# Performance work log

Measured on AMD Instinct MI355X. Metric: run time of the kernel, lower is better.

Reference implementation:

```python
import jax, jax.numpy as jnp
import numpy as np

INPUT = 27
HIDDEN = 1


def setup_inputs() -> dict:
    key = jax.random.key(0)
    k_x, k_wih, k_whh, k_bih, k_bhh = jax.random.split(key, 5)
    s = 1.0 / np.sqrt(HIDDEN)  # PyTorch LSTM init range
    x = jax.random.normal(k_x, (2048, 512, INPUT), dtype=jnp.float32)
    W_ih = jax.random.uniform(k_wih, (4 * HIDDEN, INPUT), minval=-s, maxval=s, dtype=jnp.float32)
    W_hh = jax.random.uniform(k_whh, (4 * HIDDEN, HIDDEN), minval=-s, maxval=s, dtype=jnp.float32)
    b_ih = jax.random.uniform(k_bih, (4 * HIDDEN,), minval=-s, maxval=s, dtype=jnp.float32)
    b_hh = jax.random.uniform(k_bhh, (4 * HIDDEN,), minval=-s, maxval=s, dtype=jnp.float32)
    return {"x": x, "W_ih": W_ih, "W_hh": W_hh, "b_ih": b_ih, "b_hh": b_hh}


def reference(x, W_ih, W_hh, b_ih, b_hh):
    # x: (T, B, 27). Single-layer LSTM, hidden_size=1, PyTorch gate order i,f,g,o.
    T, B, _ = x.shape
    H = HIDDEN
    # Precompute the input projection for all timesteps: (T, B, 4H)
    x_proj = jnp.einsum('tbi,gi->tbg', x, W_ih) + b_ih + b_hh

    def step(carry, xp_t):
        h, c = carry  # (B, H) each
        gates = xp_t + h @ W_hh.T  # (B, 4H)
        i = jax.nn.sigmoid(gates[:, 0 * H:1 * H])
        f = jax.nn.sigmoid(gates[:, 1 * H:2 * H])
        g = jnp.tanh(gates[:, 2 * H:3 * H])
        o = jax.nn.sigmoid(gates[:, 3 * H:4 * H])
        c_new = f * c + i * g
        h_new = o * jnp.tanh(c_new)
        return (h_new, c_new), h_new

    h0 = jnp.zeros((B, H), dtype=x.dtype)
    c0 = jnp.zeros((B, H), dtype=x.dtype)
    _, hs = jax.lax.scan(step, (h0, c0), x_proj)
    return hs  # (T, B, H)
```

## Files before the change

kernel.cpp:

```cpp
#include <hip/hip_runtime.h>

#define T_LEN 2048
#define B_SZ  512
#define NIN   27

__device__ __forceinline__ float fast_exp2(float x) { return __builtin_amdgcn_exp2f(x); }
__device__ __forceinline__ float fast_rcp(float x)  { return __builtin_amdgcn_rcpf(x); }

#define L2E 1.4426950408889634f

__global__ __launch_bounds__(256) void lstm_proj(const float* __restrict__ x,
                                                 const float* __restrict__ Wih,
                                                 const float* __restrict__ bih,
                                                 const float* __restrict__ bhh,
                                                 float4* __restrict__ A) {
    __shared__ float xs[256 * NIN];
    const int tid  = threadIdx.x;
    const size_t pos0 = (size_t)blockIdx.x * 256;

    const float4* src4 = (const float4*)(x + pos0 * NIN);
    float4* lds4 = (float4*)xs;
#pragma unroll
    for (int i = 0; i < 6; ++i) lds4[tid + i * 256] = src4[tid + i * 256];
    {
        int idx = tid + 6 * 256;
        if (idx < (256 * NIN) / 4) lds4[idx] = src4[idx];
    }

    float wreg[4 * NIN];
#pragma unroll
    for (int i = 0; i < NIN; ++i) ((float4*)wreg)[i] = ((const float4*)Wih)[i];

    float acc0 = bih[0] + bhh[0];
    float acc1 = bih[1] + bhh[1];
    float acc2 = bih[2] + bhh[2];
    float acc3 = bih[3] + bhh[3];

    __syncthreads();

    const float* xr = xs + tid * NIN;
#pragma unroll
    for (int k = 0; k < NIN; ++k) {
        float xv = xr[k];
        acc0 = fmaf(xv, wreg[0 * NIN + k], acc0);
        acc1 = fmaf(xv, wreg[1 * NIN + k], acc1);
        acc2 = fmaf(xv, wreg[2 * NIN + k], acc2);
        acc3 = fmaf(xv, wreg[3 * NIN + k], acc3);
    }

    float4 o;
    o.x = -L2E * acc0;
    o.y = -L2E * acc1;
    o.z = -2.f * L2E * acc2;
    o.w = -L2E * acc3;
    A[pos0 + tid] = o;
}

#define LSTM_STEP(a4, tt)                                                     \
    {                                                                         \
        float pi = fmaf(h, wi, (a4).x);                                       \
        float pf = fmaf(h, wf, (a4).y);                                       \
        float pg = fmaf(h, wg, (a4).z);                                       \
        float po = fmaf(h, wo, (a4).w);                                       \
        float ri = fast_rcp(1.f + fast_exp2(pi));           \
        float rf = fast_rcp(1.f + fast_exp2(pf));           \
        float rg = fast_rcp(1.f + fast_exp2(pg));         \
        float ro = fast_rcp(1.f + fast_exp2(po));           \
        float g  = fmaf(rg, 2.f, -1.f);                        \
        c = fmaf(rf, c, ri * g);                                              \
        float rc = fast_rcp(1.f + fast_exp2(c * KN));                         \
        float th = fmaf(rc, 2.f, -1.f);                          \
        h = ro * th;                                                          \
        out[(tt) * B_SZ + b] = h;                                             \
    }

__global__ __launch_bounds__(64) void lstm_scan(const float4* __restrict__ A,
                                                const float* __restrict__ Whh,
                                                float* __restrict__ out) {
    const int b = blockIdx.x * 64 + threadIdx.x;

    const float wi = -L2E * Whh[0];
    const float wf = -L2E * Whh[1];
    const float wg = -2.f * L2E * Whh[2];
    const float wo = -L2E * Whh[3];
    const float KN = -2.f * L2E;

    float h = 0.f, c = 0.f;

    constexpr int CH = 16;
    float4 bufA[CH], bufB[CH];

#pragma unroll
    for (int j = 0; j < CH; ++j) bufA[j] = A[j * B_SZ + b];

    for (int t0 = 0; t0 < T_LEN; t0 += 2 * CH) {
#pragma unroll
        for (int j = 0; j < CH; ++j) bufB[j] = A[(t0 + CH + j) * B_SZ + b];
#pragma unroll
        for (int j = 0; j < CH; ++j) LSTM_STEP(bufA[j], t0 + j);

        if (t0 + 2 * CH < T_LEN) {
#pragma unroll
            for (int j = 0; j < CH; ++j) bufA[j] = A[(t0 + 2 * CH + j) * B_SZ + b];
        }
#pragma unroll
        for (int j = 0; j < CH; ++j) LSTM_STEP(bufB[j], t0 + CH + j);
    }
}

extern "C" void kernel_launch(void* const* d_in, const int* in_sizes, int n_in,
                              void* d_out, int out_size, void* d_ws, size_t ws_size,
                              hipStream_t stream) {
    const float* x   = (const float*)d_in[0];
    const float* Wih = (const float*)d_in[1];
    const float* Whh = (const float*)d_in[2];
    const float* bih = (const float*)d_in[3];
    const float* bhh = (const float*)d_in[4];
    float* out = (float*)d_out;
    float4* A  = (float4*)d_ws;

    const int npos = T_LEN * B_SZ;
    lstm_proj<<<npos / 256, 256, 0, stream>>>(x, Wih, bih, bhh, A);
    lstm_scan<<<B_SZ / 64, 64, 0, stream>>>(A, Whh, out);
}
```

Baseline: 331.8 us.

## Stage scan gate inputs through LDS via async global-to-LDS loads

New measurement: 356.6 us. 1.07x slower.

```diff
diff --git a/kernel.cpp b/kernel.cpp
--- a/kernel.cpp
+++ b/kernel.cpp
@@ -8,6 +8,11 @@
 __device__ __forceinline__ float fast_rcp(float x)  { return __builtin_amdgcn_rcpf(x); }
 
 #define L2E 1.4426950408889634f
+
+#define GLDS(gptr, lptr)                                                          \
+    __builtin_amdgcn_global_load_lds(                                             \
+        (const __attribute__((address_space(1))) unsigned int*)(gptr),            \
+        (__attribute__((address_space(3))) unsigned int*)(lptr), 16, 0, 0)
 
 __global__ __launch_bounds__(256) void lstm_proj(const float* __restrict__ x,
                                                  const float* __restrict__ Wih,
@@ -56,6 +61,8 @@
     A[pos0 + tid] = o;
 }
 
+#define CH 32
+
 #define LSTM_STEP(a4, tt)                                                     \
     {                                                                         \
         float pi = fmaf(h, wi, (a4).x);                                       \
@@ -77,7 +84,9 @@
 __global__ __launch_bounds__(64) void lstm_scan(const float4* __restrict__ A,
                                                 const float* __restrict__ Whh,
                                                 float* __restrict__ out) {
-    const int b = blockIdx.x * 64 + threadIdx.x;
+    __shared__ float4 lds[2][CH][64];
+    const int lane = threadIdx.x;
+    const int b = (blockIdx.x << 6) + lane;
 
     const float wi = -L2E * Whh[0];
     const float wf = -L2E * Whh[1];
@@ -87,24 +96,47 @@
 
     float h = 0.f, c = 0.f;
 
-    constexpr int CH = 16;
-    float4 bufA[CH], bufB[CH];
+    const float4* Ab = A + b;
 
 #pragma unroll
-    for (int j = 0; j < CH; ++j) bufA[j] = A[j * B_SZ + b];
+    for (int j = 0; j < CH; ++j) GLDS(Ab + (size_t)j * B_SZ, &lds[0][j][0]);
+#pragma unroll
+    for (int j = 0; j < CH; ++j) GLDS(Ab + (size_t)(CH + j) * B_SZ, &lds[1][j][0]);
 
-    for (int t0 = 0; t0 < T_LEN; t0 += 2 * CH) {
+    for (int n = 0; n < T_LEN / CH; ++n) {
+        const int t0  = n * CH;
+        const int buf = n & 1;
+
+        asm volatile("s_waitcnt vmcnt(32)" ::: "memory");
+        __builtin_amdgcn_sched_barrier(0);
+
+        float4 ra[8], rb[8];
 #pragma unroll
-        for (int j = 0; j < CH; ++j) bufB[j] = A[(t0 + CH + j) * B_SZ + b];
+        for (int j = 0; j < 8; ++j) ra[j] = lds[buf][j][lane];
+
 #pragma unroll
-        for (int j = 0; j < CH; ++j) LSTM_STEP(bufA[j], t0 + j);
+        for (int j = 0; j < 8; ++j) rb[j] = lds[buf][8 + j][lane];
+#pragma unroll
+        for (int j = 0; j < 8; ++j) LSTM_STEP(ra[j], t0 + j);
+
+#pragma unroll
+        for (int j = 0; j < 8; ++j) ra[j] = lds[buf][16 + j][lane];
+#pragma unroll
+        for (int j = 0; j < 8; ++j) LSTM_STEP(rb[j], t0 + 8 + j);
+
+#pragma unroll
+        for (int j = 0; j < 8; ++j) rb[j] = lds[buf][24 + j][lane];
+#pragma unroll
+        for (int j = 0; j < 8; ++j) LSTM_STEP(ra[j], t0 + 16 + j);
+
+#pragma unroll
+        for (int j = 0; j < 8; ++j) LSTM_STEP(rb[j], t0 + 24 + j);
 
         if (t0 + 2 * CH < T_LEN) {
 #pragma unroll
-            for (int j = 0; j < CH; ++j) bufA[j] = A[(t0 + 2 * CH + j) * B_SZ + b];
+            for (int j = 0; j < CH; ++j)
+                GLDS(Ab + (size_t)(t0 + 2 * CH + j) * B_SZ, &lds[buf][j][0]);
         }
-#pragma unroll
-        for (int j = 0; j < CH; ++j) LSTM_STEP(bufB[j], t0 + CH + j);
     }
 }
 
```

## Spread LSTM gates across quad lanes with DPP broadcasts in scan kernel

Applied to the files above, without the earlier changes.

Measured after the change: 338.6 us. +2.1%, slower.

```diff
diff --git a/kernel.cpp b/kernel.cpp
--- a/kernel.cpp
+++ b/kernel.cpp
@@ -8,13 +8,22 @@
 __device__ __forceinline__ float fast_rcp(float x)  { return __builtin_amdgcn_rcpf(x); }
 
 #define L2E 1.4426950408889634f
+#define KN  (-2.0f * L2E)
+
+template<int K>
+__device__ __forceinline__ float qbcast(float v) {
+    constexpr int ctrl = K | (K << 2) | (K << 4) | (K << 6);
+    return __int_as_float(
+        __builtin_amdgcn_update_dpp(0, __float_as_int(v), ctrl, 0xf, 0xf, true));
+}
 
 __global__ __launch_bounds__(256) void lstm_proj(const float* __restrict__ x,
                                                  const float* __restrict__ Wih,
                                                  const float* __restrict__ bih,
                                                  const float* __restrict__ bhh,
                                                  float4* __restrict__ A) {
-    __shared__ float xs[256 * NIN];
+    __shared__ float  xs[256 * NIN];
+    __shared__ float4 wT[NIN];
     const int tid  = threadIdx.x;
     const size_t pos0 = (size_t)blockIdx.x * 256;
 
@@ -27,9 +36,10 @@
         if (idx < (256 * NIN) / 4) lds4[idx] = src4[idx];
     }
 
-    float wreg[4 * NIN];
-#pragma unroll
-    for (int i = 0; i < NIN; ++i) ((float4*)wreg)[i] = ((const float4*)Wih)[i];
+    if (tid < NIN) {
+        wT[tid] = make_float4(Wih[0 * NIN + tid], Wih[1 * NIN + tid],
+                              Wih[2 * NIN + tid], Wih[3 * NIN + tid]);
+    }
 
     float acc0 = bih[0] + bhh[0];
     float acc1 = bih[1] + bhh[1];
@@ -39,13 +49,14 @@
     __syncthreads();
 
     const float* xr = xs + tid * NIN;
-#pragma unroll
+#pragma unroll 3
     for (int k = 0; k < NIN; ++k) {
-        float xv = xr[k];
-        acc0 = fmaf(xv, wreg[0 * NIN + k], acc0);
-        acc1 = fmaf(xv, wreg[1 * NIN + k], acc1);
-        acc2 = fmaf(xv, wreg[2 * NIN + k], acc2);
-        acc3 = fmaf(xv, wreg[3 * NIN + k], acc3);
+        float  xv = xr[k];
+        float4 w  = wT[k];
+        acc0 = fmaf(xv, w.x, acc0);
+        acc1 = fmaf(xv, w.y, acc1);
+        acc2 = fmaf(xv, w.z, acc2);
+        acc3 = fmaf(xv, w.w, acc3);
     }
 
     float4 o;
@@ -56,55 +67,70 @@
     A[pos0 + tid] = o;
 }
 
-#define LSTM_STEP(a4, tt)                                                     \
+#define CH 16
+#define NCHUNK (T_LEN / CH)
+
+#define SCAN_STEP(vnext, tt)                                                  \
     {                                                                         \
-        float pi = fmaf(h, wi, (a4).x);                                       \
-        float pf = fmaf(h, wf, (a4).y);                                       \
-        float pg = fmaf(h, wg, (a4).z);                                       \
-        float po = fmaf(h, wo, (a4).w);                                       \
-        float ri = fast_rcp(1.f + fast_exp2(pi));           \
-        float rf = fast_rcp(1.f + fast_exp2(pf));           \
-        float rg = fast_rcp(1.f + fast_exp2(pg));         \
-        float ro = fast_rcp(1.f + fast_exp2(po));           \
-        float g  = fmaf(rg, 2.f, -1.f);                        \
-        c = fmaf(rf, c, ri * g);                                              \
-        float rc = fast_rcp(1.f + fast_exp2(c * KN));                         \
-        float th = fmaf(rc, 2.f, -1.f);                          \
-        h = ro * th;                                                          \
-        out[(tt) * B_SZ + b] = h;                                             \
+        float e   = fast_exp2(pre);                                           \
+        float r   = fast_rcp(e + 1.0f);                                       \
+        float rv  = fmaf(r, S1, S0);                                          \
+        float m_g  = qbcast<2>(rv);                                           \
+        float m_i  = qbcast<0>(rv);                                           \
+        float m_f  = qbcast<1>(rv);                                           \
+        float m_o2 = qbcast<3>(rv);                                           \
+        C = fmaf(m_f, C, m_i * m_g);                                          \
+        float e2 = fast_exp2(C);                                              \
+        float r2 = fast_rcp(e2 + 1.0f);                                       \
+        float wm = W * m_o2;                          \
+        float a2 = fmaf(wm, -0.5f, (vnext));                                  \
+        float h  = m_o2 * (r2 - 0.5f);                                        \
+        if (g == 0) out[(tt) * B_SZ + b] = h;                                 \
+        pre = fmaf(wm, r2, a2);                                               \
     }
 
-__global__ __launch_bounds__(64) void lstm_scan(const float4* __restrict__ A,
-                                                const float* __restrict__ Whh,
-                                                float* __restrict__ out) {
-    const int b = blockIdx.x * 64 + threadIdx.x;
+__global__ __launch_bounds__(64, 1) void lstm_scan(const float* __restrict__ Af,
+                                                   const float* __restrict__ Whh,
+                                                   float* __restrict__ out) {
+    const int lane = threadIdx.x;
+    const int g    = lane & 3;
+    const int b    = (blockIdx.x << 4) + (lane >> 2);
 
-    const float wi = -L2E * Whh[0];
-    const float wf = -L2E * Whh[1];
-    const float wg = -2.f * L2E * Whh[2];
-    const float wo = -L2E * Whh[3];
-    const float KN = -2.f * L2E;
+    const float* src = Af + (size_t)(blockIdx.x << 6) + lane;
 
-    float h = 0.f, c = 0.f;
+    const float sg = (g == 2) ? (-2.f * L2E) : (-L2E);
+    const float W  = sg * Whh[g];
+    const float S1 = (g == 0) ? KN : ((g == 1) ? 1.f : 2.f);
+    const float S0 = (g == 2) ? -1.f : 0.f;
 
-    constexpr int CH = 16;
-    float4 bufA[CH], bufB[CH];
+    float C = 0.f;
+
+    float pa[CH], pb[CH];
 
 #pragma unroll
-    for (int j = 0; j < CH; ++j) bufA[j] = A[j * B_SZ + b];
+    for (int j = 0; j < CH; ++j) pa[j] = src[(size_t)j * 2048];
+    float pre = pa[0];
 
-    for (int t0 = 0; t0 < T_LEN; t0 += 2 * CH) {
+    for (int n = 0; n < NCHUNK; n += 2) {
+        const int t0 = n * CH;
+
 #pragma unroll
-        for (int j = 0; j < CH; ++j) bufB[j] = A[(t0 + CH + j) * B_SZ + b];
+        for (int j = 0; j < CH; ++j) pb[j] = src[(size_t)(t0 + CH + j) * 2048];
+        __builtin_amdgcn_sched_barrier(0);
+
 #pragma unroll
-        for (int j = 0; j < CH; ++j) LSTM_STEP(bufA[j], t0 + j);
+        for (int j = 0; j < CH - 1; ++j) SCAN_STEP(pa[j + 1], t0 + j);
+        SCAN_STEP(pb[0], t0 + CH - 1);
 
-        if (t0 + 2 * CH < T_LEN) {
+        if (n + 2 < NCHUNK) {
 #pragma unroll
-            for (int j = 0; j < CH; ++j) bufA[j] = A[(t0 + 2 * CH + j) * B_SZ + b];
+            for (int j = 0; j < CH; ++j) pa[j] = src[(size_t)(t0 + 2 * CH + j) * 2048];
         }
+        __builtin_amdgcn_sched_barrier(0);
+
 #pragma unroll
-        for (int j = 0; j < CH; ++j) LSTM_STEP(bufB[j], t0 + CH + j);
+        for (int j = 0; j < CH - 1; ++j) SCAN_STEP(pb[j + 1], t0 + CH + j);
+        SCAN_STEP(pa[0], t0 + 2 * CH - 1);
     }
 }
 
@@ -121,5 +147,5 @@
 
     const int npos = T_LEN * B_SZ;
     lstm_proj<<<npos / 256, 256, 0, stream>>>(x, Wih, bih, bhh, A);
-    lstm_scan<<<B_SZ / 64, 64, 0, stream>>>(A, Whh, out);
+    lstm_scan<<<B_SZ / 16, 64, 0, stream>>>((const float*)A, Whh, out);
 }
```
